# Performance work log

Measured on AMD Instinct MI355X. Metric: run time of the kernel, lower is better.

## Reference

```python
import jax, jax.numpy as jnp
import numpy as np

B, S, D, H = 2, 2048, 1024, 16
HD = D // H  # head_dim = 64


def setup_inputs() -> dict:
    key = jax.random.key(0)
    ks = jax.random.split(key, 5)
    scale = 1.0 / np.sqrt(D)
    return {
        "x": jax.random.normal(ks[0], (B, S, D), dtype=jnp.float32),
        "w_qkv": jax.random.normal(ks[1], (D, 3 * D), dtype=jnp.float32) * scale,
        "b_qkv": jnp.zeros((3 * D,), dtype=jnp.float32),
        "w_out": jax.random.normal(ks[2], (D, D), dtype=jnp.float32) * scale,
        "b_out": jnp.zeros((D,), dtype=jnp.float32),
    }


def reference(x, w_qkv, b_qkv, w_out, b_out):
    b, s, d = x.shape
    qkv = x @ w_qkv + b_qkv  # [B,S,3D]
    q, k, v = jnp.split(qkv, 3, axis=-1)
    # [B,S,D] -> [B,H,S,HD]
    def to_heads(t):
        return t.reshape(b, s, H, HD).transpose(0, 2, 1, 3)
    q, k, v = to_heads(q), to_heads(k), to_heads(v)
    scores = jnp.einsum("bhqd,bhkd->bhqk", q, k) / np.sqrt(HD)
    attn = jax.nn.softmax(scores, axis=-1)
    out = jnp.einsum("bhqk,bhkd->bhqd", attn, v)  # [B,H,S,HD]
    out = out.transpose(0, 2, 1, 3).reshape(b, s, d)
    return out @ w_out + b_out
```

## Files before the change

kernel.cpp:

```cpp
#include <hip/hip_runtime.h>
#include <hip/hip_bf16.h>
#include <math.h>


typedef __bf16 bf16;
typedef __attribute__((ext_vector_type(8))) __bf16 bf16x8;
typedef __attribute__((ext_vector_type(4))) __bf16 bf16x4;
typedef __attribute__((ext_vector_type(4))) float f32x4;

#define B_ 2
#define S_ 2048
#define D_ 1024
#define H_ 16
#define HD_ 64

__device__ __forceinline__ f32x4 mfma16(bf16x8 a, bf16x8 b, f32x4 c) {
    return __builtin_amdgcn_mfma_f32_16x16x32_bf16(a, b, c, 0, 0, 0);
}

__device__ __forceinline__ void gload_lds16(const void* g, void* l) {
    __builtin_amdgcn_global_load_lds(
        (const __attribute__((address_space(1))) void*)g,
        (__attribute__((address_space(3))) void*)l, 16, 0, 0);
}

__device__ __forceinline__ bf16x8 pack8(const f32x4 a, const f32x4 b) {
    union { bf16x8 v; __hip_bfloat162 h[4]; } u;
    u.h[0] = __float22bfloat162_rn(make_float2(a[0], a[1]));
    u.h[1] = __float22bfloat162_rn(make_float2(a[2], a[3]));
    u.h[2] = __float22bfloat162_rn(make_float2(b[0], b[1]));
    u.h[3] = __float22bfloat162_rn(make_float2(b[2], b[3]));
    return u.v;
}


__global__ __launch_bounds__(256) void convert_x_kernel(
        const float* __restrict__ x, bf16* __restrict__ xb) {
    int i = blockIdx.x * 256 + threadIdx.x;
    float4 v = ((const float4*)x)[i];
    bf16x4 o = { (bf16)v.x, (bf16)v.y, (bf16)v.z, (bf16)v.w };
    ((bf16x4*)xb)[i] = o;
}

__global__ __launch_bounds__(256) void transpose_w_kernel(
        const float* __restrict__ src, bf16* __restrict__ dst, int K, int N,
        float scale, int scale_cols) {
    __shared__ bf16 Ls[64 * 65];
    const int t = threadIdx.x;
    const int n0 = blockIdx.x * 64, k0 = blockIdx.y * 64;
    const float sc = (n0 < scale_cols) ? scale : 1.0f;
    for (int p = 0; p < 4; p++) {
        int r = p * 16 + (t >> 4);
        int c4 = (t & 15) * 4;
        float4 v = *(const float4*)&src[(size_t)(k0 + r) * N + n0 + c4];
        Ls[r * 65 + c4 + 0] = (bf16)(v.x * sc);
        Ls[r * 65 + c4 + 1] = (bf16)(v.y * sc);
        Ls[r * 65 + c4 + 2] = (bf16)(v.z * sc);
        Ls[r * 65 + c4 + 3] = (bf16)(v.w * sc);
    }
    __syncthreads();
    for (int p = 0; p < 4; p++) {
        int nl = p * 16 + (t >> 4);
        int kc = (t & 15) * 4;
        bf16x4 o = { Ls[(kc + 0) * 65 + nl], Ls[(kc + 1) * 65 + nl],
                     Ls[(kc + 2) * 65 + nl], Ls[(kc + 3) * 65 + nl] };
        *(bf16x4*)&dst[(size_t)(n0 + nl) * K + k0 + kc] = o;
    }
}

template <bool OUT_BF16>
__global__ __launch_bounds__(256) void gemm_bt_kernel(
        const bf16* __restrict__ A, const bf16* __restrict__ Bt,
        const float* __restrict__ bias, void* __restrict__ Cout,
        int M, int N, int K, float bias_scale, int bias_cols) {
    __shared__ bf16 As[128 * 32];
    __shared__ bf16 Bs[128 * 32];
    const int t = threadIdx.x;
    const int lane = t & 63, w = t >> 6;
    const int g = lane >> 4, c = lane & 15;
    const int m0 = blockIdx.y * 128, n0 = blockIdx.x * 128;
    const int wm = (w >> 1) * 64, wn = (w & 1) * 64;

    f32x4 acc[4][4];
    for (int i = 0; i < 4; i++)
        for (int j = 0; j < 4; j++) acc[i][j] = (f32x4){0.f, 0.f, 0.f, 0.f};

    const size_t rowB = (size_t)K * 2;
    const char* Abase = (const char*)A + (size_t)m0 * rowB;
    const char* Bbase = (const char*)Bt + (size_t)n0 * rowB;

    for (int kt = 0; kt < K; kt += 32) {
        for (int i = 0; i < 2; i++) {
            int boff = (w * 2 + i) * 1024 + lane * 16;
            int row = boff >> 6;
            int colb = boff & 63;
            gload_lds16(Abase + (size_t)row * rowB + (size_t)kt * 2 + colb,
                        (char*)As + (w * 2 + i) * 1024);
            gload_lds16(Bbase + (size_t)row * rowB + (size_t)kt * 2 + colb,
                        (char*)Bs + (w * 2 + i) * 1024);
        }
        __syncthreads();
        bf16x8 af[4], bfr[4];
        for (int mt = 0; mt < 4; mt++)
            af[mt] = *(const bf16x8*)&As[(wm + mt * 16 + c) * 32 + g * 8];
        for (int nt = 0; nt < 4; nt++)
            bfr[nt] = *(const bf16x8*)&Bs[(wn + nt * 16 + c) * 32 + g * 8];
        for (int mt = 0; mt < 4; mt++)
            for (int nt = 0; nt < 4; nt++)
                acc[mt][nt] = mfma16(af[mt], bfr[nt], acc[mt][nt]);
        __syncthreads();
    }

    const float bsc = (n0 < bias_cols) ? bias_scale : 1.0f;
    for (int mt = 0; mt < 4; mt++) {
        for (int nt = 0; nt < 4; nt++) {
            int col = n0 + wn + nt * 16 + c;
            float bv = bias[col] * bsc;
            for (int r = 0; r < 4; r++) {
                int row = m0 + wm + mt * 16 + g * 4 + r;
                float v = acc[mt][nt][r] + bv;
                if (OUT_BF16)
                    ((bf16*)Cout)[(size_t)row * N + col] = (bf16)v;
                else
                    ((float*)Cout)[(size_t)row * N + col] = v;
            }
        }
    }
}

__global__ __launch_bounds__(256) void repack_v_kernel(
        const bf16* __restrict__ qkv, bf16* __restrict__ vt) {
    int bh = blockIdx.y, b = bh >> 4, h = bh & 15;
    int s0 = blockIdx.x * 64;
    int lane = threadIdx.x & 63, wv = threadIdx.x >> 6;
    int s = s0 + lane;
    const bf16* src = qkv + (size_t)(b * S_ + s) * (3 * D_) + 2 * D_ + h * HD_;
    bf16* dst = vt + (size_t)bh * HD_ * S_ + s;
    for (int i = 0; i < 16; i++) {
        int hd = wv * 16 + i;
        dst[(size_t)hd * S_] = src[hd];
    }
}

#define KT_ 64
#define KEYS_HALF_ (S_ / 2)

__global__ __launch_bounds__(512, 4) void attn_kernel(
        const bf16* __restrict__ qkv, const bf16* __restrict__ vt,
        bf16* __restrict__ out) {
    __shared__ bf16 KV[2][2][2][KT_ * HD_];
    __shared__ float Ls2[128];

    const int t = threadIdx.x;
    const int lane = t & 63, wv = t >> 6;
    const int half = wv >> 2, wvl = wv & 3;
    const int g = lane >> 4, c = lane & 15;
    const int bh = blockIdx.y, b = bh >> 4, h = bh & 15;
    const int qbase = blockIdx.x * 128 + wvl * 16;

    const bf16 onev = (bf16)1.0f;
    const bf16x8 ones = { onev, onev, onev, onev, onev, onev, onev, onev };

    bf16x8 qf[2][2];
    for (int ch = 0; ch < 2; ch++) {
        const size_t qoff = (size_t)(b * S_ + qbase + ch * 64 + c) * (3 * D_) + h * HD_;
        qf[ch][0] = *(const bf16x8*)(qkv + qoff + g * 8);
        qf[ch][1] = *(const bf16x8*)(qkv + qoff + 32 + g * 8);
    }

    f32x4 o[2][4];
    for (int ch = 0; ch < 2; ch++)
        for (int i = 0; i < 4; i++) o[ch][i] = (f32x4){0.f, 0.f, 0.f, 0.f};
    f32x4 lacc[2];
    lacc[0] = lacc[1] = (f32x4){0.f, 0.f, 0.f, 0.f};

    size_t koff[2], voff[2];
    for (int j = 0; j < 2; j++) {
        int r = wvl * 16 + j * 8 + (lane >> 3);
        int key = ((r >> 5) & 1) * 32 + ((r >> 3) & 1) * 16 +
                  ((r >> 2) & 1) * 8 + ((r >> 4) & 1) * 4 + (r & 3);
        int blk = (lane & 7) ^ (r & 7);
        koff[j] = (size_t)key * (3 * D_) + blk * 8;
        voff[j] = (size_t)r * S_ + blk * 8;
    }
    const bf16* kbase = qkv + (size_t)(b * S_ + half * KEYS_HALF_) * (3 * D_) + D_ + h * HD_;
    const bf16* vbase = vt + (size_t)bh * HD_ * S_ + half * KEYS_HALF_;

    for (int j = 0; j < 2; j++) {
        gload_lds16(kbase + koff[j], (char*)&KV[half][0][0][0] + (wvl * 2 + j) * 1024);
        gload_lds16(vbase + voff[j], (char*)&KV[half][1][0][0] + (wvl * 2 + j) * 1024);
    }
    __syncthreads();

    const int cs7 = c & 7;
    for (int tile = 0; tile < KEYS_HALF_ / KT_; tile++) {
        const int buf = tile & 1;
        if (tile + 1 < KEYS_HALF_ / KT_) {
            const int j0 = (tile + 1) * KT_;
            for (int j = 0; j < 2; j++) {
                gload_lds16(kbase + (size_t)j0 * (3 * D_) + koff[j],
                            (char*)&KV[half][0][buf ^ 1][0] + (wvl * 2 + j) * 1024);
                gload_lds16(vbase + j0 + voff[j],
                            (char*)&KV[half][1][buf ^ 1][0] + (wvl * 2 + j) * 1024);
            }
        }

        bf16x8 kf0[4], kf1[4];
        for (int kt = 0; kt < 4; kt++) {
            const bf16* row = &KV[half][0][buf][(kt * 16 + c) * 64];
            kf0[kt] = *(const bf16x8*)(row + ((g ^ cs7) * 8));
            kf1[kt] = *(const bf16x8*)(row + (((g ^ 4) ^ cs7) * 8));
        }
        bf16x8 vf0[4], vf1[4];
        for (int nt = 0; nt < 4; nt++) {
            const bf16* row = &KV[half][1][buf][(nt * 16 + c) * 64];
            vf0[nt] = *(const bf16x8*)(row + ((g ^ cs7) * 8));
            vf1[nt] = *(const bf16x8*)(row + (((g ^ 4) ^ cs7) * 8));
        }

        for (int ch = 0; ch < 2; ch++) {
            f32x4 p[4];
            for (int kt = 0; kt < 4; kt++) {
                f32x4 acc = (f32x4){0.f, 0.f, 0.f, 0.f};
                acc = mfma16(kf0[kt], qf[ch][0], acc);
                acc = mfma16(kf1[kt], qf[ch][1], acc);
                for (int r = 0; r < 4; r++)
                    p[kt][r] = __builtin_amdgcn_exp2f(acc[r]);
            }

            bf16x8 pb0 = pack8(p[0], p[1]);
            bf16x8 pb1 = pack8(p[2], p[3]);

            lacc[ch] = mfma16(ones, pb0, lacc[ch]);
            lacc[ch] = mfma16(ones, pb1, lacc[ch]);

            for (int nt = 0; nt < 4; nt++) {
                o[ch][nt] = mfma16(vf0[nt], pb0, o[ch][nt]);
                o[ch][nt] = mfma16(vf1[nt], pb1, o[ch][nt]);
            }
        }
        __syncthreads();
    }

    float* Os = (float*)&KV[1][0][0][0];
    if (half == 1) {
        for (int ch = 0; ch < 2; ch++) {
            for (int nt = 0; nt < 4; nt++)
                *(f32x4*)&Os[(((wvl * 2 + ch) * 4 + nt) * 64 + lane) * 4] = o[ch][nt];
            if (lane < 16)
                Ls2[ch * 64 + wvl * 16 + c] = lacc[ch][0];
        }
    }
    __syncthreads();
    if (half == 0) {
        for (int ch = 0; ch < 2; ch++) {
            float lh = lacc[ch][0] + Ls2[ch * 64 + wvl * 16 + c];
            float inv = 1.f / lh;
            int q = qbase + ch * 64 + c;
            size_t base = (size_t)(b * S_ + q) * D_ + h * HD_ + g * 4;
            for (int nt = 0; nt < 4; nt++) {
                f32x4 po = *(const f32x4*)&Os[(((wvl * 2 + ch) * 4 + nt) * 64 + lane) * 4];
                bf16x4 ov = { (bf16)((o[ch][nt][0] + po[0]) * inv),
                              (bf16)((o[ch][nt][1] + po[1]) * inv),
                              (bf16)((o[ch][nt][2] + po[2]) * inv),
                              (bf16)((o[ch][nt][3] + po[3]) * inv) };
                *(bf16x4*)&out[base + nt * 16] = ov;
            }
        }
    }
}


extern "C" void kernel_launch(void* const* d_in, const int* in_sizes, int n_in,
                              void* d_out, int out_size, void* d_ws, size_t ws_size,
                              hipStream_t stream) {
    const float* x     = (const float*)d_in[0];
    const float* w_qkv = (const float*)d_in[1];
    const float* b_qkv = (const float*)d_in[2];
    const float* w_out = (const float*)d_in[3];
    const float* b_out = (const float*)d_in[4];
    float* out = (float*)d_out;

    const float cs = 0.125f * 1.44269504088896341f;

    char* ws = (char*)d_ws;
    bf16* x_bf    = (bf16*)(ws + 0);
    bf16* attn_bf = x_bf;
    bf16* wqkv_t  = (bf16*)(ws + (8u << 20));
    bf16* wout_t  = (bf16*)(ws + (14u << 20));
    bf16* qkv_bf  = (bf16*)(ws + (16u << 20));
    bf16* v_t     = (bf16*)(ws + (40u << 20));

    convert_x_kernel<<<(B_ * S_ * D_) / (256 * 4), 256, 0, stream>>>(x, x_bf);
    transpose_w_kernel<<<dim3(3 * D_ / 64, D_ / 64), 256, 0, stream>>>(
        w_qkv, wqkv_t, D_, 3 * D_, cs, D_);
    transpose_w_kernel<<<dim3(D_ / 64, D_ / 64), 256, 0, stream>>>(
        w_out, wout_t, D_, D_, 1.0f, 0);

    gemm_bt_kernel<true><<<dim3(3 * D_ / 128, B_ * S_ / 128), 256, 0, stream>>>(
        x_bf, wqkv_t, b_qkv, qkv_bf, B_ * S_, 3 * D_, D_, cs, D_);

    repack_v_kernel<<<dim3(S_ / 64, B_ * H_), 256, 0, stream>>>(qkv_bf, v_t);

    attn_kernel<<<dim3(S_ / 128, B_ * H_), 512, 0, stream>>>(qkv_bf, v_t, attn_bf);

    gemm_bt_kernel<false><<<dim3(D_ / 128, B_ * S_ / 128), 256, 0, stream>>>(
        attn_bf, wout_t, b_out, out, B_ * S_, D_, D_, 1.0f, 0);
}
```

Before: 199.2 us.

## Merge prep kernels into one launch and widen GEMM K-tile with XOR swizzle

The x conversion and both weight transposes now run as one combined launch, removing two kernel launches and the gaps between them. The GEMM K-tile grows from 32 to 64, which halves the number of loads and barrier pairs per output tile. An XOR swizzle on the LDS column placement is added to avoid bank conflicts when the wider rows are read. Doubling the LDS tile size may lower occupancy, and the swizzle indexing has to match exactly between the global-to-LDS writes and the fragment reads.

```diff
diff --git a/kernel.cpp b/kernel.cpp
--- a/kernel.cpp
+++ b/kernel.cpp
@@ -33,21 +33,10 @@
     return u.v;
 }
 
-
-__global__ __launch_bounds__(256) void convert_x_kernel(
-        const float* __restrict__ x, bf16* __restrict__ xb) {
-    int i = blockIdx.x * 256 + threadIdx.x;
-    float4 v = ((const float4*)x)[i];
-    bf16x4 o = { (bf16)v.x, (bf16)v.y, (bf16)v.z, (bf16)v.w };
-    ((bf16x4*)xb)[i] = o;
-}
-
-__global__ __launch_bounds__(256) void transpose_w_kernel(
+__device__ __forceinline__ void transpose_tile(
         const float* __restrict__ src, bf16* __restrict__ dst, int K, int N,
-        float scale, int scale_cols) {
-    __shared__ bf16 Ls[64 * 65];
-    const int t = threadIdx.x;
-    const int n0 = blockIdx.x * 64, k0 = blockIdx.y * 64;
+        float scale, int scale_cols, int bx, int by, int t, bf16* Ls) {
+    const int n0 = bx * 64, k0 = by * 64;
     const float sc = (n0 < scale_cols) ? scale : 1.0f;
     for (int p = 0; p < 4; p++) {
         int r = p * 16 + (t >> 4);
@@ -68,16 +57,38 @@
     }
 }
 
+__global__ __launch_bounds__(256) void prep_kernel(
+        const float* __restrict__ x, bf16* __restrict__ xb,
+        const float* __restrict__ w_qkv, bf16* __restrict__ wqkv_t,
+        const float* __restrict__ w_out, bf16* __restrict__ wout_t,
+        float cs) {
+    __shared__ bf16 Ls[64 * 65];
+    const int bid = blockIdx.x, t = threadIdx.x;
+    if (bid < 4096) {
+        int i = bid * 256 + t;
+        float4 v = ((const float4*)x)[i];
+        bf16x4 o = { (bf16)v.x, (bf16)v.y, (bf16)v.z, (bf16)v.w };
+        ((bf16x4*)xb)[i] = o;
+    } else if (bid < 4864) {
+        int b2 = bid - 4096;
+        transpose_tile(w_qkv, wqkv_t, D_, 3 * D_, cs, D_, b2 % 48, b2 / 48, t, Ls);
+    } else {
+        int b3 = bid - 4864;
+        transpose_tile(w_out, wout_t, D_, D_, 1.0f, 0, b3 % 16, b3 / 16, t, Ls);
+    }
+}
+
 template <bool OUT_BF16>
 __global__ __launch_bounds__(256) void gemm_bt_kernel(
         const bf16* __restrict__ A, const bf16* __restrict__ Bt,
         const float* __restrict__ bias, void* __restrict__ Cout,
         int M, int N, int K, float bias_scale, int bias_cols) {
-    __shared__ bf16 As[128 * 32];
-    __shared__ bf16 Bs[128 * 32];
+    __shared__ bf16 As[128 * 64];
+    __shared__ bf16 Bs[128 * 64];
     const int t = threadIdx.x;
     const int lane = t & 63, w = t >> 6;
     const int g = lane >> 4, c = lane & 15;
+    const int c7 = c & 7;
     const int m0 = blockIdx.y * 128, n0 = blockIdx.x * 128;
     const int wm = (w >> 1) * 64, wn = (w & 1) * 64;
 
@@ -89,25 +100,35 @@
     const char* Abase = (const char*)A + (size_t)m0 * rowB;
     const char* Bbase = (const char*)Bt + (size_t)n0 * rowB;
 
-    for (int kt = 0; kt < K; kt += 32) {
-        for (int i = 0; i < 2; i++) {
-            int boff = (w * 2 + i) * 1024 + lane * 16;
-            int row = boff >> 6;
-            int colb = boff & 63;
-            gload_lds16(Abase + (size_t)row * rowB + (size_t)kt * 2 + colb,
-                        (char*)As + (w * 2 + i) * 1024);
-            gload_lds16(Bbase + (size_t)row * rowB + (size_t)kt * 2 + colb,
-                        (char*)Bs + (w * 2 + i) * 1024);
+    int srow[4], scol[4];
+    for (int i = 0; i < 4; i++) {
+        srow[i] = (w * 4 + i) * 8 + (lane >> 3);
+        scol[i] = ((lane & 7) ^ (srow[i] & 7)) * 16;
+    }
+
+    for (int kt = 0; kt < K; kt += 64) {
+        for (int i = 0; i < 4; i++) {
+            gload_lds16(Abase + (size_t)srow[i] * rowB + (size_t)kt * 2 + scol[i],
+                        (char*)As + (w * 4 + i) * 1024);
+            gload_lds16(Bbase + (size_t)srow[i] * rowB + (size_t)kt * 2 + scol[i],
+                        (char*)Bs + (w * 4 + i) * 1024);
         }
         __syncthreads();
-        bf16x8 af[4], bfr[4];
-        for (int mt = 0; mt < 4; mt++)
-            af[mt] = *(const bf16x8*)&As[(wm + mt * 16 + c) * 32 + g * 8];
-        for (int nt = 0; nt < 4; nt++)
-            bfr[nt] = *(const bf16x8*)&Bs[(wn + nt * 16 + c) * 32 + g * 8];
-        for (int mt = 0; mt < 4; mt++)
-            for (int nt = 0; nt < 4; nt++)
-                acc[mt][nt] = mfma16(af[mt], bfr[nt], acc[mt][nt]);
+        for (int kh = 0; kh < 2; kh++) {
+            const int xb = (kh * 4);
+            bf16x8 af[4], bfr[4];
+            for (int mt = 0; mt < 4; mt++) {
+                int row = wm + mt * 16 + c;
+                af[mt] = *(const bf16x8*)&As[row * 64 + (((xb + g) ^ c7)) * 8];
+            }
+            for (int nt = 0; nt < 4; nt++) {
+                int row = wn + nt * 16 + c;
+                bfr[nt] = *(const bf16x8*)&Bs[row * 64 + (((xb + g) ^ c7)) * 8];
+            }
+            for (int mt = 0; mt < 4; mt++)
+                for (int nt = 0; nt < 4; nt++)
+                    acc[mt][nt] = mfma16(af[mt], bfr[nt], acc[mt][nt]);
+        }
         __syncthreads();
     }
 
@@ -291,11 +312,7 @@
     bf16* qkv_bf  = (bf16*)(ws + (16u << 20));
     bf16* v_t     = (bf16*)(ws + (40u << 20));
 
-    convert_x_kernel<<<(B_ * S_ * D_) / (256 * 4), 256, 0, stream>>>(x, x_bf);
-    transpose_w_kernel<<<dim3(3 * D_ / 64, D_ / 64), 256, 0, stream>>>(
-        w_qkv, wqkv_t, D_, 3 * D_, cs, D_);
-    transpose_w_kernel<<<dim3(D_ / 64, D_ / 64), 256, 0, stream>>>(
-        w_out, wout_t, D_, D_, 1.0f, 0);
+    prep_kernel<<<5120, 256, 0, stream>>>(x, x_bf, w_qkv, wqkv_t, w_out, wout_t, cs);
 
     gemm_bt_kernel<true><<<dim3(3 * D_ / 128, B_ * S_ / 128), 256, 0, stream>>>(
         x_bf, wqkv_t, b_qkv, qkv_bf, B_ * S_, 3 * D_, D_, cs, D_);
```

After: 187.5 us. 1.06x faster.
